# Kernel tuning notes

Measured on AMD Instinct MI355X. Metric: run time of the kernel, lower is better.

Reference implementation:

```python
import jax, jax.numpy as jnp
import numpy as np

COMMITMENT_COST = 0.25
K, D = 1024, 64          # num_embeddings, embedding_dim
B, T = 32, 4096          # batch, tokens per batch element


def setup_inputs() -> dict:
    key = jax.random.key(0)
    k1, k2 = jax.random.split(key)
    inputs = jax.random.normal(k1, (B, T, D), dtype=jnp.float32)
    # xavier_uniform over [K, D]: bound = sqrt(6/(K+D))
    bound = float(np.sqrt(6.0 / (K + D)))
    embedding = jax.random.uniform(k2, (K, D), dtype=jnp.float32,
                                   minval=-bound, maxval=bound)
    return {"inputs": inputs, "embedding": embedding}


def reference(inputs, embedding):
    input_shape = inputs.shape
    flat = inputs.reshape(-1, embedding.shape[1])            # [N, D]
    input_sq = jnp.sum(flat ** 2, axis=1, keepdims=True)     # [N, 1]
    embed_sq = jnp.sum(embedding ** 2, axis=1)               # [K]
    dot = flat @ embedding.T                                 # [N, K]
    distances = input_sq + embed_sq - 2.0 * dot              # [N, K]
    idx = jnp.argmin(distances, axis=1)                      # [N]
    quant = embedding[idx]                                   # [N, D]
    q_latent_loss = jnp.mean((quant - jax.lax.stop_gradient(flat)) ** 2)
    e_latent_loss = jnp.mean((jax.lax.stop_gradient(quant) - flat) ** 2)
    loss = q_latent_loss + COMMITMENT_COST * e_latent_loss
    # straight-through estimator
    quant_st = flat + jax.lax.stop_gradient(quant - flat)
    quant_st = quant_st.reshape(input_shape)
    encoding_indices = idx.reshape(input_shape[0], -1)
    return quant_st, loss, encoding_indices
```

## Files before the change

### kernel.cpp

```cpp
#include <hip/hip_runtime.h>


#define KC 1024
#define DD 64
#define NTOK (32 * 4096)
#define QUANT_ELEMS ((size_t)NTOK * DD)
#define LOSS_OFF QUANT_ELEMS
#define IDX_OFF (QUANT_ELEMS + 1)

#define WS_E2 0
#define WS_BFRAG_F 2048
#define WS_BSUM (WS_BFRAG_F + 65536)

#define DIST_BLOCKS (NTOK / 128)

typedef _Float16 f16x8 __attribute__((ext_vector_type(8)));
typedef float f32x4 __attribute__((ext_vector_type(4)));

__device__ __forceinline__ unsigned int sortable_bits(float f) {
  unsigned int b = __float_as_uint(f);
  return b ^ (unsigned int)(((int)b >> 31) | 0x80000000);
}

__device__ __forceinline__ float unsortable_bits(unsigned int u) {
  unsigned int fb = (u & 0x80000000u) ? (u ^ 0x80000000u) : ~u;
  return __uint_as_float(fb);
}

__device__ __forceinline__ float row_sumsq_np8(const float* p) {
  float r[8];
#pragma unroll
  for (int j = 0; j < 8; ++j) r[j] = p[j] * p[j];
#pragma unroll
  for (int i = 1; i < 8; ++i)
#pragma unroll
    for (int j = 0; j < 8; ++j) {
      float v = p[i * 8 + j];
      r[j] += v * v;
    }
  return ((r[0] + r[1]) + (r[2] + r[3])) + ((r[4] + r[5]) + (r[6] + r[7]));
}

__global__ void vq_setup(const float* __restrict__ emb,
                         float* __restrict__ ws) {
  const int b = blockIdx.x;
  const int tid = threadIdx.x;
  if (b < 64) {
    const int nt = b;
    const int f = tid >> 6;
    const int lane = tid & 63;
    const int plane = f >> 1, ks = f & 1;
    const int n = nt * 16 + (lane & 15);
    const int kb = ks * 32 + ((lane >> 4) & 3) * 8;
    const float* ep = emb + (size_t)n * DD + kb;
    f16x8 o;
#pragma unroll
    for (int j = 0; j < 8; ++j) {
      float v = ep[j];
      _Float16 h = (_Float16)v;
      o[j] = (plane == 0) ? h : (_Float16)(v - (float)h);
    }
    ((f16x8*)(ws + WS_BFRAG_F))[(nt * 4 + f) * 64 + lane] = o;
  } else {
    const int k = (b - 64) * 256 + tid;
    ws[WS_E2 + k] = row_sumsq_np8(emb + (size_t)k * DD);
  }
}

__launch_bounds__(256, 2)
__global__ void vq_dist_mfma(const float* __restrict__ x_in,
                             const float* __restrict__ emb,
                             const float* __restrict__ ws_ro,
                             float* __restrict__ out,
                             float* __restrict__ blocksum) {
  const int tid = threadIdx.x;
  const int wave = tid >> 6, lane = tid & 63;
  const int quad = lane >> 4, l16 = lane & 15;
  const int tokBase = blockIdx.x * 128 + wave * 32;

  __shared__ float4 Bf[2][1024];
  __shared__ float E2s[KC];
  __shared__ float x2s[128];
  __shared__ float wsum[4];

  const float4* bsrc = (const float4*)(ws_ro + WS_BFRAG_F);

  float4 st[4];
#pragma unroll
  for (int i = 0; i < 4; ++i) st[i] = bsrc[i * 256 + tid];
#pragma unroll
  for (int i = 0; i < 4; ++i)
    E2s[i * 256 + tid] = ws_ro[WS_E2 + i * 256 + tid];

  if (lane < 32)
    x2s[wave * 32 + lane] =
        row_sumsq_np8(x_in + (size_t)(tokBase + lane) * DD);

  f16x8 ah[2][2], al[2][2];
#pragma unroll
  for (int ms = 0; ms < 2; ++ms) {
    const float* xr = x_in + (size_t)(tokBase + ms * 16 + l16) * DD;
#pragma unroll
    for (int ks = 0; ks < 2; ++ks) {
      const float4* p = (const float4*)(xr + ks * 32 + quad * 8);
      float4 v0 = p[0], v1 = p[1];
      float vv[8] = {v0.x, v0.y, v0.z, v0.w, v1.x, v1.y, v1.z, v1.w};
#pragma unroll
      for (int j = 0; j < 8; ++j) {
        _Float16 h = (_Float16)vv[j];
        ah[ms][ks][j] = h;
        al[ms][ks][j] = (_Float16)(vv[j] - (float)h);
      }
    }
  }

#pragma unroll
  for (int i = 0; i < 4; ++i) Bf[0][i * 256 + tid] = st[i];

  float best[2][4];
  int bidx[2][4];
#pragma unroll
  for (int ms = 0; ms < 2; ++ms)
#pragma unroll
    for (int r = 0; r < 4; ++r) { best[ms][r] = 3.402823466e38f; bidx[ms][r] = 0; }

  __syncthreads();

  float x2v[2][4];
#pragma unroll
  for (int ms = 0; ms < 2; ++ms)
#pragma unroll
    for (int r = 0; r < 4; ++r)
      x2v[ms][r] = x2s[wave * 32 + ms * 16 + quad * 4 + r];

  for (int q = 0; q < 16; ++q) {
    const int buf = q & 1;
    if (q < 15) {
#pragma unroll
      for (int i = 0; i < 4; ++i)
        st[i] = bsrc[(q + 1) * 1024 + i * 256 + tid];
    }
    const f16x8* bfp = (const f16x8*)Bf[buf];
#pragma unroll
    for (int lt = 0; lt < 4; ++lt) {
      const int ch = lt * 4;
      f16x8 bh0 = bfp[(ch + 0) * 64 + lane];
      f16x8 bh1 = bfp[(ch + 1) * 64 + lane];
      f16x8 bl0 = bfp[(ch + 2) * 64 + lane];
      f16x8 bl1 = bfp[(ch + 3) * 64 + lane];
      const int ncur = q * 64 + lt * 16 + l16;
      const float e2v = E2s[ncur];
      f32x4 acc[2];
#pragma unroll
      for (int ms = 0; ms < 2; ++ms) acc[ms] = (f32x4){0.f, 0.f, 0.f, 0.f};
#pragma unroll
      for (int ms = 0; ms < 2; ++ms)
        acc[ms] = __builtin_amdgcn_mfma_f32_16x16x32_f16(ah[ms][0], bh0, acc[ms], 0, 0, 0);
#pragma unroll
      for (int ms = 0; ms < 2; ++ms)
        acc[ms] = __builtin_amdgcn_mfma_f32_16x16x32_f16(ah[ms][1], bh1, acc[ms], 0, 0, 0);
#pragma unroll
      for (int ms = 0; ms < 2; ++ms)
        acc[ms] = __builtin_amdgcn_mfma_f32_16x16x32_f16(al[ms][0], bh0, acc[ms], 0, 0, 0);
#pragma unroll
      for (int ms = 0; ms < 2; ++ms)
        acc[ms] = __builtin_amdgcn_mfma_f32_16x16x32_f16(al[ms][1], bh1, acc[ms], 0, 0, 0);
#pragma unroll
      for (int ms = 0; ms < 2; ++ms)
        acc[ms] = __builtin_amdgcn_mfma_f32_16x16x32_f16(ah[ms][0], bl0, acc[ms], 0, 0, 0);
#pragma unroll
      for (int ms = 0; ms < 2; ++ms)
        acc[ms] = __builtin_amdgcn_mfma_f32_16x16x32_f16(ah[ms][1], bl1, acc[ms], 0, 0, 0);
#pragma unroll
      for (int ms = 0; ms < 2; ++ms)
#pragma unroll
        for (int r = 0; r < 4; ++r) {
          float s = __builtin_fmaf(-2.0f, acc[ms][r], x2v[ms][r] + e2v);
          if (s < best[ms][r]) { best[ms][r] = s; bidx[ms][r] = ncur; }
        }
    }
    if (q < 15) {
#pragma unroll
      for (int i = 0; i < 4; ++i) Bf[buf ^ 1][i * 256 + tid] = st[i];
    }
    __syncthreads();
  }

  unsigned long long key[2][4];
#pragma unroll
  for (int ms = 0; ms < 2; ++ms)
#pragma unroll
    for (int r = 0; r < 4; ++r) {
      unsigned long long k =
          ((unsigned long long)sortable_bits(best[ms][r]) << 32) |
          (unsigned int)bidx[ms][r];
#pragma unroll
      for (int m = 1; m < 16; m <<= 1) {
        unsigned long long o = __shfl_xor(k, m);
        k = o < k ? o : k;
      }
      key[ms][r] = k;
    }

  float qsum = 0.0f;
#pragma unroll
  for (int ms = 0; ms < 2; ++ms)
#pragma unroll
    for (int r = 0; r < 4; ++r) {
      const int token = tokBase + ms * 16 + quad * 4 + r;
      const int widx = (int)(unsigned int)key[ms][r];
      if (l16 == 0) out[IDX_OFF + (size_t)token] = (float)widx;
      const float4 v = ((const float4*)(emb + (size_t)widx * DD))[l16];
      ((float4*)(out + (size_t)token * DD))[l16] = v;
      qsum += unsortable_bits((unsigned int)(key[ms][r] >> 32));
    }

  float tot = __shfl(qsum, 0) + __shfl(qsum, 16) +
              __shfl(qsum, 32) + __shfl(qsum, 48);
  if (lane == 0) wsum[wave] = tot;
  __syncthreads();
  if (tid == 0)
    blocksum[blockIdx.x] = (wsum[0] + wsum[1]) + (wsum[2] + wsum[3]);
}

__global__ void vq_finish(const float* __restrict__ blocksum,
                          float* __restrict__ out) {
  const int tid = threadIdx.x;
  float s = 0.0f;
#pragma unroll
  for (int i = 0; i < DIST_BLOCKS / 256; ++i)
    s += blocksum[i * 256 + tid];
#pragma unroll
  for (int off = 32; off > 0; off >>= 1) s += __shfl_down(s, off);
  __shared__ float wsum[4];
  const int wid = tid >> 6;
  if ((tid & 63) == 0) wsum[wid] = s;
  __syncthreads();
  if (tid == 0) {
    float total = (wsum[0] + wsum[1]) + (wsum[2] + wsum[3]);
    float m = total / (float)QUANT_ELEMS;
    out[LOSS_OFF] = m + 0.25f * m;
  }
}

extern "C" void kernel_launch(void* const* d_in, const int* in_sizes, int n_in,
                              void* d_out, int out_size, void* d_ws, size_t ws_size,
                              hipStream_t stream) {
  const float* x = (const float*)d_in[0];
  const float* emb = (const float*)d_in[1];
  float* out = (float*)d_out;
  float* ws = (float*)d_ws;

  vq_setup<<<68, 256, 0, stream>>>(emb, ws);
  vq_dist_mfma<<<DIST_BLOCKS, 256, 0, stream>>>(x, emb, ws, out, ws + WS_BSUM);
  vq_finish<<<1, 256, 0, stream>>>(ws + WS_BSUM, out);
}
```

Before: 137.7 us.

## Fuse codebook fp16 split into main kernel with per-block multi-pass staging

Removes the separate setup kernel. Each 512-thread block now converts the fp32 codebook into hi/lo fp16 MFMA fragments itself, in four passes of 256 codes each, and computes all codebook squared norms locally. Blocks double in token count (256 tokens, 8 waves) and launch bounds rise to 4 blocks per CU. This saves one kernel launch and the workspace round trip, but every block redundantly recomputes the codebook conversion and norms. The earlier global-to-LDS double buffering is replaced by synchronous rebuilds between passes, which stall the MFMA loop.

```diff
diff --git a/kernel.cpp b/kernel.cpp
--- a/kernel.cpp
+++ b/kernel.cpp
@@ -8,11 +8,10 @@
 #define LOSS_OFF QUANT_ELEMS
 #define IDX_OFF (QUANT_ELEMS + 1)
 
-#define WS_E2 0
-#define WS_BFRAG_F 2048
-#define WS_BSUM (WS_BFRAG_F + 65536)
-
-#define DIST_BLOCKS (NTOK / 128)
+#define MAIN_BLOCKS (NTOK / 256)
+#define NPASS 4
+#define CODES_PP (KC / NPASS)
+#define TILES_PP (CODES_PP / 16)
 
 typedef _Float16 f16x8 __attribute__((ext_vector_type(8)));
 typedef float f32x4 __attribute__((ext_vector_type(4)));
@@ -41,57 +40,49 @@
   return ((r[0] + r[1]) + (r[2] + r[3])) + ((r[4] + r[5]) + (r[6] + r[7]));
 }
 
-__global__ void vq_setup(const float* __restrict__ emb,
-                         float* __restrict__ ws) {
-  const int b = blockIdx.x;
-  const int tid = threadIdx.x;
-  if (b < 64) {
-    const int nt = b;
-    const int f = tid >> 6;
-    const int lane = tid & 63;
-    const int plane = f >> 1, ks = f & 1;
-    const int n = nt * 16 + (lane & 15);
-    const int kb = ks * 32 + ((lane >> 4) & 3) * 8;
-    const float* ep = emb + (size_t)n * DD + kb;
-    f16x8 o;
-#pragma unroll
-    for (int j = 0; j < 8; ++j) {
-      float v = ep[j];
-      _Float16 h = (_Float16)v;
-      o[j] = (plane == 0) ? h : (_Float16)(v - (float)h);
-    }
-    ((f16x8*)(ws + WS_BFRAG_F))[(nt * 4 + f) * 64 + lane] = o;
-  } else {
-    const int k = (b - 64) * 256 + tid;
-    ws[WS_E2 + k] = row_sumsq_np8(emb + (size_t)k * DD);
-  }
-}
-
-__launch_bounds__(256, 2)
-__global__ void vq_dist_mfma(const float* __restrict__ x_in,
-                             const float* __restrict__ emb,
-                             const float* __restrict__ ws_ro,
-                             float* __restrict__ out,
-                             float* __restrict__ blocksum) {
+__launch_bounds__(512, 4)
+__global__ void vq_main(const float* __restrict__ x_in,
+                        const float* __restrict__ emb,
+                        float* __restrict__ out,
+                        float* __restrict__ blocksum) {
   const int tid = threadIdx.x;
   const int wave = tid >> 6, lane = tid & 63;
   const int quad = lane >> 4, l16 = lane & 15;
-  const int tokBase = blockIdx.x * 128 + wave * 32;
-
-  __shared__ float4 Bf[2][1024];
+  const int tokBase = blockIdx.x * 256 + wave * 32;
+
+  __shared__ f16x8 Bl[TILES_PP * 4 * 64];
   __shared__ float E2s[KC];
-  __shared__ float x2s[128];
-  __shared__ float wsum[4];
-
-  const float4* bsrc = (const float4*)(ws_ro + WS_BFRAG_F);
-
-  float4 st[4];
-#pragma unroll
-  for (int i = 0; i < 4; ++i) st[i] = bsrc[i * 256 + tid];
-#pragma unroll
-  for (int i = 0; i < 4; ++i)
-    E2s[i * 256 + tid] = ws_ro[WS_E2 + i * 256 + tid];
-
+  __shared__ float x2s[256];
+  __shared__ float wsum[8];
+
+  auto build_B = [&](int p) {
+#pragma unroll
+    for (int t = 0; t < 4; ++t) {
+      const int idx = t * 512 + tid;
+      const int nl = idx >> 3;
+      const int c = idx & 7;
+      const int ks = c >> 2;
+      const int ln = (nl & 15) | ((c & 3) << 4);
+      const int nt = nl >> 4;
+      const float4* src =
+          (const float4*)(emb + (size_t)(p * CODES_PP + nl) * DD + c * 8);
+      float4 v0 = src[0], v1 = src[1];
+      float vv[8] = {v0.x, v0.y, v0.z, v0.w, v1.x, v1.y, v1.z, v1.w};
+      f16x8 oh, ol;
+#pragma unroll
+      for (int j = 0; j < 8; ++j) {
+        _Float16 h = (_Float16)vv[j];
+        oh[j] = h;
+        ol[j] = (_Float16)(vv[j] - (float)h);
+      }
+      Bl[(nt * 4 + ks) * 64 + ln] = oh;
+      Bl[(nt * 4 + 2 + ks) * 64 + ln] = ol;
+    }
+  };
+
+  build_B(0);
+  E2s[tid] = row_sumsq_np8(emb + (size_t)tid * DD);
+  E2s[512 + tid] = row_sumsq_np8(emb + (size_t)(512 + tid) * DD);
   if (lane < 32)
     x2s[wave * 32 + lane] =
         row_sumsq_np8(x_in + (size_t)(tokBase + lane) * DD);
@@ -102,8 +93,8 @@
     const float* xr = x_in + (size_t)(tokBase + ms * 16 + l16) * DD;
 #pragma unroll
     for (int ks = 0; ks < 2; ++ks) {
-      const float4* p = (const float4*)(xr + ks * 32 + quad * 8);
-      float4 v0 = p[0], v1 = p[1];
+      const float4* p4 = (const float4*)(xr + ks * 32 + quad * 8);
+      float4 v0 = p4[0], v1 = p4[1];
       float vv[8] = {v0.x, v0.y, v0.z, v0.w, v1.x, v1.y, v1.z, v1.w};
 #pragma unroll
       for (int j = 0; j < 8; ++j) {
@@ -114,9 +105,6 @@
     }
   }
 
-#pragma unroll
-  for (int i = 0; i < 4; ++i) Bf[0][i * 256 + tid] = st[i];
-
   float best[2][4];
   int bidx[2][4];
 #pragma unroll
@@ -133,22 +121,15 @@
     for (int r = 0; r < 4; ++r)
       x2v[ms][r] = x2s[wave * 32 + ms * 16 + quad * 4 + r];
 
-  for (int q = 0; q < 16; ++q) {
-    const int buf = q & 1;
-    if (q < 15) {
-#pragma unroll
-      for (int i = 0; i < 4; ++i)
-        st[i] = bsrc[(q + 1) * 1024 + i * 256 + tid];
-    }
-    const f16x8* bfp = (const f16x8*)Bf[buf];
-#pragma unroll
-    for (int lt = 0; lt < 4; ++lt) {
+  for (int p = 0; p < NPASS; ++p) {
+#pragma unroll 4
+    for (int lt = 0; lt < TILES_PP; ++lt) {
       const int ch = lt * 4;
-      f16x8 bh0 = bfp[(ch + 0) * 64 + lane];
-      f16x8 bh1 = bfp[(ch + 1) * 64 + lane];
-      f16x8 bl0 = bfp[(ch + 2) * 64 + lane];
-      f16x8 bl1 = bfp[(ch + 3) * 64 + lane];
-      const int ncur = q * 64 + lt * 16 + l16;
+      f16x8 bh0 = Bl[(ch + 0) * 64 + lane];
+      f16x8 bh1 = Bl[(ch + 1) * 64 + lane];
+      f16x8 bl0 = Bl[(ch + 2) * 64 + lane];
+      f16x8 bl1 = Bl[(ch + 3) * 64 + lane];
+      const int ncur = p * CODES_PP + lt * 16 + l16;
       const float e2v = E2s[ncur];
       f32x4 acc[2];
 #pragma unroll
@@ -179,11 +160,11 @@
           if (s < best[ms][r]) { best[ms][r] = s; bidx[ms][r] = ncur; }
         }
     }
-    if (q < 15) {
-#pragma unroll
-      for (int i = 0; i < 4; ++i) Bf[buf ^ 1][i * 256 + tid] = st[i];
-    }
-    __syncthreads();
+    if (p < NPASS - 1) {
+      __syncthreads();
+      build_B(p + 1);
+      __syncthreads();
+    }
   }
 
   unsigned long long key[2][4];
@@ -220,16 +201,14 @@
   if (lane == 0) wsum[wave] = tot;
   __syncthreads();
   if (tid == 0)
-    blocksum[blockIdx.x] = (wsum[0] + wsum[1]) + (wsum[2] + wsum[3]);
+    blocksum[blockIdx.x] = ((wsum[0] + wsum[1]) + (wsum[2] + wsum[3])) +
+                           ((wsum[4] + wsum[5]) + (wsum[6] + wsum[7]));
 }
 
 __global__ void vq_finish(const float* __restrict__ blocksum,
                           float* __restrict__ out) {
   const int tid = threadIdx.x;
-  float s = 0.0f;
-#pragma unroll
-  for (int i = 0; i < DIST_BLOCKS / 256; ++i)
-    s += blocksum[i * 256 + tid];
+  float s = blocksum[tid] + blocksum[256 + tid];
 #pragma unroll
   for (int off = 32; off > 0; off >>= 1) s += __shfl_down(s, off);
   __shared__ float wsum[4];
@@ -251,7 +230,6 @@
   float* out = (float*)d_out;
   float* ws = (float*)d_ws;
 
-  vq_setup<<<68, 256, 0, stream>>>(emb, ws);
-  vq_dist_mfma<<<DIST_BLOCKS, 256, 0, stream>>>(x, emb, ws, out, ws + WS_BSUM);
-  vq_finish<<<1, 256, 0, stream>>>(ws + WS_BSUM, out);
-}
+  vq_main<<<MAIN_BLOCKS, 512, 0, stream>>>(x, emb, out, ws);
+  vq_finish<<<1, 256, 0, stream>>>(ws, out);
+}
```

New measurement: 147.6 us. +7.3%, slower.

## Double token tile per wave and stream codebook fragments from global into registers

Applied to the files above, without the earlier changes.

Each wave now handles 64 tokens instead of 32, so every codebook fragment load feeds four MFMA row tiles instead of two. The LDS double-buffered codebook staging and its per-chunk __syncthreads are removed; B fragments are read straight from global/L2 into registers with a two-deep software prefetch. MFMA bursts are wrapped in s_setprio. The block count halves to 512, which lowers parallelism, and the larger register footprint may hurt occupancy under the 256x2 launch bound.

```diff
diff --git a/kernel.cpp b/kernel.cpp
--- a/kernel.cpp
+++ b/kernel.cpp
@@ -12,7 +12,7 @@
 #define WS_BFRAG_F 2048
 #define WS_BSUM (WS_BFRAG_F + 65536)
 
-#define DIST_BLOCKS (NTOK / 128)
+#define MAIN_BLOCKS (NTOK / 256)
 
 typedef _Float16 f16x8 __attribute__((ext_vector_type(8)));
 typedef float f32x4 __attribute__((ext_vector_type(4)));
@@ -68,42 +68,33 @@
 }
 
 __launch_bounds__(256, 2)
-__global__ void vq_dist_mfma(const float* __restrict__ x_in,
-                             const float* __restrict__ emb,
-                             const float* __restrict__ ws_ro,
-                             float* __restrict__ out,
-                             float* __restrict__ blocksum) {
+__global__ void vq_main(const float* __restrict__ x_in,
+                        const float* __restrict__ emb,
+                        const float* __restrict__ ws_ro,
+                        float* __restrict__ out,
+                        float* __restrict__ blocksum) {
   const int tid = threadIdx.x;
   const int wave = tid >> 6, lane = tid & 63;
   const int quad = lane >> 4, l16 = lane & 15;
-  const int tokBase = blockIdx.x * 128 + wave * 32;
-
-  __shared__ float4 Bf[2][1024];
+  const int tokBase = blockIdx.x * 256 + wave * 64;
+
   __shared__ float E2s[KC];
-  __shared__ float x2s[128];
+  __shared__ float x2s[256];
   __shared__ float wsum[4];
 
-  const float4* bsrc = (const float4*)(ws_ro + WS_BFRAG_F);
-
-  float4 st[4];
-#pragma unroll
-  for (int i = 0; i < 4; ++i) st[i] = bsrc[i * 256 + tid];
 #pragma unroll
   for (int i = 0; i < 4; ++i)
     E2s[i * 256 + tid] = ws_ro[WS_E2 + i * 256 + tid];
-
-  if (lane < 32)
-    x2s[wave * 32 + lane] =
-        row_sumsq_np8(x_in + (size_t)(tokBase + lane) * DD);
-
-  f16x8 ah[2][2], al[2][2];
-#pragma unroll
-  for (int ms = 0; ms < 2; ++ms) {
+  x2s[wave * 64 + lane] = row_sumsq_np8(x_in + (size_t)(tokBase + lane) * DD);
+
+  f16x8 ah[4][2], al[4][2];
+#pragma unroll
+  for (int ms = 0; ms < 4; ++ms) {
     const float* xr = x_in + (size_t)(tokBase + ms * 16 + l16) * DD;
 #pragma unroll
     for (int ks = 0; ks < 2; ++ks) {
-      const float4* p = (const float4*)(xr + ks * 32 + quad * 8);
-      float4 v0 = p[0], v1 = p[1];
+      const float4* p4 = (const float4*)(xr + ks * 32 + quad * 8);
+      float4 v0 = p4[0], v1 = p4[1];
       float vv[8] = {v0.x, v0.y, v0.z, v0.w, v1.x, v1.y, v1.z, v1.w};
 #pragma unroll
       for (int j = 0; j < 8; ++j) {
@@ -114,81 +105,77 @@
     }
   }
 
-#pragma unroll
-  for (int i = 0; i < 4; ++i) Bf[0][i * 256 + tid] = st[i];
-
-  float best[2][4];
-  int bidx[2][4];
-#pragma unroll
-  for (int ms = 0; ms < 2; ++ms)
+  float best[4][4];
+  int bidx[4][4];
+#pragma unroll
+  for (int ms = 0; ms < 4; ++ms)
 #pragma unroll
     for (int r = 0; r < 4; ++r) { best[ms][r] = 3.402823466e38f; bidx[ms][r] = 0; }
 
   __syncthreads();
 
-  float x2v[2][4];
-#pragma unroll
-  for (int ms = 0; ms < 2; ++ms)
+  float x2v[4][4];
+#pragma unroll
+  for (int ms = 0; ms < 4; ++ms)
 #pragma unroll
     for (int r = 0; r < 4; ++r)
-      x2v[ms][r] = x2s[wave * 32 + ms * 16 + quad * 4 + r];
-
-  for (int q = 0; q < 16; ++q) {
-    const int buf = q & 1;
-    if (q < 15) {
-#pragma unroll
-      for (int i = 0; i < 4; ++i)
-        st[i] = bsrc[(q + 1) * 1024 + i * 256 + tid];
-    }
-    const f16x8* bfp = (const f16x8*)Bf[buf];
-#pragma unroll
-    for (int lt = 0; lt < 4; ++lt) {
-      const int ch = lt * 4;
-      f16x8 bh0 = bfp[(ch + 0) * 64 + lane];
-      f16x8 bh1 = bfp[(ch + 1) * 64 + lane];
-      f16x8 bl0 = bfp[(ch + 2) * 64 + lane];
-      f16x8 bl1 = bfp[(ch + 3) * 64 + lane];
-      const int ncur = q * 64 + lt * 16 + l16;
-      const float e2v = E2s[ncur];
-      f32x4 acc[2];
-#pragma unroll
-      for (int ms = 0; ms < 2; ++ms) acc[ms] = (f32x4){0.f, 0.f, 0.f, 0.f};
-#pragma unroll
-      for (int ms = 0; ms < 2; ++ms)
-        acc[ms] = __builtin_amdgcn_mfma_f32_16x16x32_f16(ah[ms][0], bh0, acc[ms], 0, 0, 0);
-#pragma unroll
-      for (int ms = 0; ms < 2; ++ms)
-        acc[ms] = __builtin_amdgcn_mfma_f32_16x16x32_f16(ah[ms][1], bh1, acc[ms], 0, 0, 0);
-#pragma unroll
-      for (int ms = 0; ms < 2; ++ms)
-        acc[ms] = __builtin_amdgcn_mfma_f32_16x16x32_f16(al[ms][0], bh0, acc[ms], 0, 0, 0);
-#pragma unroll
-      for (int ms = 0; ms < 2; ++ms)
-        acc[ms] = __builtin_amdgcn_mfma_f32_16x16x32_f16(al[ms][1], bh1, acc[ms], 0, 0, 0);
-#pragma unroll
-      for (int ms = 0; ms < 2; ++ms)
-        acc[ms] = __builtin_amdgcn_mfma_f32_16x16x32_f16(ah[ms][0], bl0, acc[ms], 0, 0, 0);
-#pragma unroll
-      for (int ms = 0; ms < 2; ++ms)
-        acc[ms] = __builtin_amdgcn_mfma_f32_16x16x32_f16(ah[ms][1], bl1, acc[ms], 0, 0, 0);
-#pragma unroll
-      for (int ms = 0; ms < 2; ++ms)
-#pragma unroll
-        for (int r = 0; r < 4; ++r) {
-          float s = __builtin_fmaf(-2.0f, acc[ms][r], x2v[ms][r] + e2v);
-          if (s < best[ms][r]) { best[ms][r] = s; bidx[ms][r] = ncur; }
-        }
-    }
-    if (q < 15) {
-#pragma unroll
-      for (int i = 0; i < 4; ++i) Bf[buf ^ 1][i * 256 + tid] = st[i];
-    }
-    __syncthreads();
-  }
-
-  unsigned long long key[2][4];
-#pragma unroll
-  for (int ms = 0; ms < 2; ++ms)
+      x2v[ms][r] = x2s[wave * 64 + ms * 16 + quad * 4 + r];
+
+  const f16x8* bws = (const f16x8*)(ws_ro + WS_BFRAG_F);
+
+  auto compute = [&](int nt, const f16x8 (&bf)[4]) {
+    const int ncur = nt * 16 + l16;
+    const float e2v = E2s[ncur];
+    f32x4 acc[4];
+#pragma unroll
+    for (int ms = 0; ms < 4; ++ms) acc[ms] = (f32x4){0.f, 0.f, 0.f, 0.f};
+    __builtin_amdgcn_s_setprio(1);
+#pragma unroll
+    for (int ms = 0; ms < 4; ++ms)
+      acc[ms] = __builtin_amdgcn_mfma_f32_16x16x32_f16(ah[ms][0], bf[0], acc[ms], 0, 0, 0);
+#pragma unroll
+    for (int ms = 0; ms < 4; ++ms)
+      acc[ms] = __builtin_amdgcn_mfma_f32_16x16x32_f16(ah[ms][1], bf[1], acc[ms], 0, 0, 0);
+#pragma unroll
+    for (int ms = 0; ms < 4; ++ms)
+      acc[ms] = __builtin_amdgcn_mfma_f32_16x16x32_f16(al[ms][0], bf[0], acc[ms], 0, 0, 0);
+#pragma unroll
+    for (int ms = 0; ms < 4; ++ms)
+      acc[ms] = __builtin_amdgcn_mfma_f32_16x16x32_f16(al[ms][1], bf[1], acc[ms], 0, 0, 0);
+#pragma unroll
+    for (int ms = 0; ms < 4; ++ms)
+      acc[ms] = __builtin_amdgcn_mfma_f32_16x16x32_f16(ah[ms][0], bf[2], acc[ms], 0, 0, 0);
+#pragma unroll
+    for (int ms = 0; ms < 4; ++ms)
+      acc[ms] = __builtin_amdgcn_mfma_f32_16x16x32_f16(ah[ms][1], bf[3], acc[ms], 0, 0, 0);
+    __builtin_amdgcn_s_setprio(0);
+#pragma unroll
+    for (int ms = 0; ms < 4; ++ms)
+#pragma unroll
+      for (int r = 0; r < 4; ++r) {
+        float s = __builtin_fmaf(-2.0f, acc[ms][r], x2v[ms][r] + e2v);
+        if (s < best[ms][r]) { best[ms][r] = s; bidx[ms][r] = ncur; }
+      }
+  };
+
+  f16x8 bA[4], bB[4];
+#pragma unroll
+  for (int i = 0; i < 4; ++i) bA[i] = bws[i * 64 + lane];
+
+  for (int nt = 0; nt < 64; nt += 2) {
+#pragma unroll
+    for (int i = 0; i < 4; ++i) bB[i] = bws[((nt + 1) * 4 + i) * 64 + lane];
+    compute(nt, bA);
+    if (nt + 2 < 64) {
+#pragma unroll
+      for (int i = 0; i < 4; ++i) bA[i] = bws[((nt + 2) * 4 + i) * 64 + lane];
+    }
+    compute(nt + 1, bB);
+  }
+
+  unsigned long long key[4][4];
+#pragma unroll
+  for (int ms = 0; ms < 4; ++ms)
 #pragma unroll
     for (int r = 0; r < 4; ++r) {
       unsigned long long k =
@@ -204,7 +191,7 @@
 
   float qsum = 0.0f;
 #pragma unroll
-  for (int ms = 0; ms < 2; ++ms)
+  for (int ms = 0; ms < 4; ++ms)
 #pragma unroll
     for (int r = 0; r < 4; ++r) {
       const int token = tokBase + ms * 16 + quad * 4 + r;
@@ -226,10 +213,7 @@
 __global__ void vq_finish(const float* __restrict__ blocksum,
                           float* __restrict__ out) {
   const int tid = threadIdx.x;
-  float s = 0.0f;
-#pragma unroll
-  for (int i = 0; i < DIST_BLOCKS / 256; ++i)
-    s += blocksum[i * 256 + tid];
+  float s = blocksum[tid] + blocksum[256 + tid];
 #pragma unroll
   for (int off = 32; off > 0; off >>= 1) s += __shfl_down(s, off);
   __shared__ float wsum[4];
@@ -252,6 +236,6 @@
   float* ws = (float*)d_ws;
 
   vq_setup<<<68, 256, 0, stream>>>(emb, ws);
-  vq_dist_mfma<<<DIST_BLOCKS, 256, 0, stream>>>(x, emb, ws, out, ws + WS_BSUM);
+  vq_main<<<MAIN_BLOCKS, 256, 0, stream>>>(x, emb, ws, out, ws + WS_BSUM);
   vq_finish<<<1, 256, 0, stream>>>(ws + WS_BSUM, out);
 }
```

After: 138.7 us. About the same (+0.8%).
